# Kernel tuning notes

Measured on AMD Instinct MI355X. Metric: run time of the kernel, lower is better.

Reference implementation:

```python
import jax, jax.numpy as jnp
import numpy as np
from jax import lax

H = 64  # LSTM units (hard-coded in the module)


def _lstm(x, W, U, b, return_sequences):
    """Keras-style LSTM (inference; recurrent_dropout inactive).
    x: [B, T, F]; W: [F, 4H]; U: [H, 4H]; b: [4H].
    Gate order (Keras): i, f, g(cell), o.
    """
    B = x.shape[0]
    # Precompute input contribution for all timesteps: [T, B, 4H]
    xz = jnp.einsum('btf,fg->tbg', x, W) + b

    def step(carry, z_t):
        h, c = carry
        z = z_t + h @ U  # [B, 4H]
        i = jax.nn.sigmoid(z[:, :H])
        f = jax.nn.sigmoid(z[:, H:2 * H])
        g = jnp.tanh(z[:, 2 * H:3 * H])
        o = jax.nn.sigmoid(z[:, 3 * H:])
        c = f * c + i * g
        h = o * jnp.tanh(c)
        return (h, c), h

    init = (jnp.zeros((B, H), x.dtype), jnp.zeros((B, H), x.dtype))
    (h_last, _), hs = lax.scan(step, init, xz)
    if return_sequences:
        return jnp.transpose(hs, (1, 0, 2))  # [B, T, H]
    return h_last  # [B, H]


def setup_inputs() -> dict:
    key = jax.random.key(0)
    ks = jax.random.split(key, 8)
    B, T, F = 4096, 256, 32
    s_in = 1.0 / np.sqrt(F)
    s_h = 1.0 / np.sqrt(H)
    return {
        'x': jax.random.normal(ks[0], (B, T, F), jnp.float32),
        'W1': jax.random.normal(ks[1], (F, 4 * H), jnp.float32) * s_in,
        'U1': jax.random.normal(ks[2], (H, 4 * H), jnp.float32) * s_h,
        'b1': jnp.zeros((4 * H,), jnp.float32),
        'W2': jax.random.normal(ks[3], (H, 4 * H), jnp.float32) * s_h,
        'U2': jax.random.normal(ks[4], (H, 4 * H), jnp.float32) * s_h,
        'b2': jnp.zeros((4 * H,), jnp.float32),
        'Wd': jax.random.normal(ks[5], (H, H), jnp.float32) * s_h,
        'bd': jnp.zeros((H,), jnp.float32),
        'Wo': jax.random.normal(ks[6], (H, 1), jnp.float32) * s_h,
        'bo': jnp.zeros((1,), jnp.float32),
    }


def reference(x, W1, U1, b1, W2, U2, b2, Wd, bd, Wo, bo):
    h_seq = _lstm(x, W1, U1, b1, return_sequences=True)   # hidden_lstm
    h_last = _lstm(h_seq, W2, U2, b2, return_sequences=False)  # lstm_layer
    d = jax.nn.sigmoid(h_last @ Wd + bd)  # Dense(64, sigmoid)
    return jax.nn.sigmoid(d @ Wo + bo)    # Dense(1, sigmoid) -> [B, 1]
```

## Files before the change

kernel.cpp:

```cpp
#include <hip/hip_runtime.h>


typedef __attribute__((ext_vector_type(8))) short short8;
typedef __attribute__((ext_vector_type(4))) float floatx4;
typedef __attribute__((ext_vector_type(2))) float floatx2;

__device__ __forceinline__ float ex2(float x){ return __builtin_amdgcn_exp2f(x); }
__device__ __forceinline__ float rcp_(float x){ return __builtin_amdgcn_rcpf(x); }
__device__ __forceinline__ float sigm(float x){ return rcp_(1.0f + ex2(-1.44269504f*x)); }
__device__ __forceinline__ unsigned bfbits(float f){
    unsigned u = __builtin_bit_cast(unsigned, f);
    u += 0x7FFFu + ((u >> 16) & 1u);
    return u >> 16;
}
__device__ __forceinline__ short f2bf(float f){ return (short)bfbits(f); }
__device__ __forceinline__ unsigned pack_bf2(float a, float b){
    return bfbits(a) | (bfbits(b) << 16);
}

#define MFMA_BF16 __builtin_amdgcn_mfma_f32_16x16x32_bf16

__global__ __launch_bounds__(512, 1)
void lstm2_pipe(const float* __restrict__ x,
                const float* __restrict__ W1, const float* __restrict__ U1, const float* __restrict__ b1,
                const float* __restrict__ W2, const float* __restrict__ U2, const float* __restrict__ b2,
                const float* __restrict__ Wd, const float* __restrict__ bd,
                const float* __restrict__ Wo, const float* __restrict__ bo,
                float* __restrict__ out)
{
    __shared__ __align__(16) short h1b[2][16 * 72];
    __shared__ __align__(16) short h2b[2][16 * 72];
    __shared__ __align__(16) short xsb[2][16 * 40];
    __shared__ float psum[4][16];

    const int tid  = threadIdx.x;
    const int w    = tid >> 6;
    const bool isA = (w < 4);
    const int wv   = isA ? w : (w - 4);
    const int lane = tid & 63;
    const int m    = lane & 15;
    const int q    = lane >> 4;
    const int b0   = blockIdx.x * 16;
    const int col  = wv * 16 + m;

    const float LG  = 1.44269504f;

    short8 Wf[16];
    float  bg[4];
    if (isA) {
#pragma unroll
        for (int g = 0; g < 4; ++g) {
            const float s = (g == 2) ? (2.0f * LG) : (-LG);
            const int n = g * 64 + col;
            bg[g] = b1[n] * s;
#pragma unroll
            for (int j = 0; j < 8; ++j) {
                const int k = q * 8 + j;
                Wf[g * 3 + 0][j] = f2bf(W1[k * 256 + n] * s);
                Wf[g * 3 + 1][j] = f2bf(U1[k * 256 + n] * s);
                Wf[g * 3 + 2][j] = f2bf(U1[(32 + k) * 256 + n] * s);
            }
        }
    } else {
#pragma unroll
        for (int g = 0; g < 4; ++g) {
            const float s = (g == 2) ? (2.0f * LG) : (-LG);
            const int n = g * 64 + col;
            bg[g] = b2[n] * s;
#pragma unroll
            for (int j = 0; j < 8; ++j) {
                const int k = q * 8 + j;
                Wf[g * 4 + 0][j] = f2bf(W2[k * 256 + n] * s);
                Wf[g * 4 + 1][j] = f2bf(W2[(32 + k) * 256 + n] * s);
                Wf[g * 4 + 2][j] = f2bf(U2[k * 256 + n] * s);
                Wf[g * 4 + 3][j] = f2bf(U2[(32 + k) * 256 + n] * s);
            }
        }
    }

    {
        unsigned* p1 = (unsigned*)&h1b[0][0];
        unsigned* p2 = (unsigned*)&h2b[0][0];
        for (int i = tid; i < 1152; i += 512) { p1[i] = 0u; p2[i] = 0u; }
    }

    const int xr = tid >> 4;
    const int xc = (tid & 15) * 2;
    const float* xrow = x + (size_t)(b0 + xr) * 8192 + xc;
    floatx2 xv0;
    if (isA) {
        floatx2 v = *(const floatx2*)xrow;
        *(unsigned*)&xsb[0][xr * 40 + xc] = pack_bf2(v.x, v.y);
        xv0 = *(const floatx2*)(xrow + 32);
    }
    __syncthreads();

    float c[4] = {0, 0, 0, 0};

    for (int u = 0; u <= 256; ++u) {
        const int par = u & 1, pax = par ^ 1;
        if (isA) {
            if (u < 256) {
                short8 a0 = *(const short8*)&xsb[par][m * 40 + q * 8];
                short8 a1 = *(const short8*)&h1b[pax][m * 72 + q * 8];
                short8 a2 = *(const short8*)&h1b[pax][m * 72 + 32 + q * 8];
                floatx4 z[4];
#pragma unroll
                for (int g = 0; g < 4; ++g) {
                    floatx4 acc = { bg[g], bg[g], bg[g], bg[g] };
                    acc = MFMA_BF16(a0, Wf[g * 3 + 0], acc, 0, 0, 0);
                    acc = MFMA_BF16(a1, Wf[g * 3 + 1], acc, 0, 0, 0);
                    acc = MFMA_BF16(a2, Wf[g * 3 + 2], acc, 0, 0, 0);
                    z[g] = acc;
                }
                float hv[4];
#pragma unroll
                for (int r = 0; r < 4; ++r) {
                    float iv = rcp_(1.0f + ex2(z[0][r]));
                    float fv = rcp_(1.0f + ex2(z[1][r]));
                    float rg = rcp_(1.0f + ex2(z[2][r]));
                    float ov = rcp_(1.0f + ex2(z[3][r]));
                    float gp = fmaf(-5.77078016f, rg, 2.88539008f);
                    c[r] = fmaf(fv, c[r], iv * gp);
                    float th = fmaf(-2.0f, rcp_(1.0f + ex2(c[r])), 1.0f);
                    hv[r] = ov * th;
                }
                unsigned p01 = pack_bf2(hv[0], hv[1]);
                unsigned p23 = pack_bf2(hv[2], hv[3]);
                short* hw = &h1b[par][(q * 4) * 72 + col];
                hw[0]       = (short)(p01 & 0xFFFF);
                hw[72]      = (short)(p01 >> 16);
                hw[144]     = (short)(p23 & 0xFFFF);
                hw[216]     = (short)(p23 >> 16);
                if (u < 255) {
                    *(unsigned*)&xsb[pax][xr * 40 + xc] = pack_bf2(xv0.x, xv0.y);
                    if (u < 254) xv0 = *(const floatx2*)(xrow + (size_t)(u + 2) * 32);
                }
            }
        } else {
            if (u >= 1) {
                short8 g0 = *(const short8*)&h1b[pax][m * 72 + q * 8];
                short8 g1 = *(const short8*)&h1b[pax][m * 72 + 32 + q * 8];
                short8 g2 = *(const short8*)&h2b[par][m * 72 + q * 8];
                short8 g3 = *(const short8*)&h2b[par][m * 72 + 32 + q * 8];
                floatx4 z[4];
#pragma unroll
                for (int g = 0; g < 4; ++g) {
                    floatx4 acc = { bg[g], bg[g], bg[g], bg[g] };
                    acc = MFMA_BF16(g0, Wf[g * 4 + 0], acc, 0, 0, 0);
                    acc = MFMA_BF16(g1, Wf[g * 4 + 1], acc, 0, 0, 0);
                    acc = MFMA_BF16(g2, Wf[g * 4 + 2], acc, 0, 0, 0);
                    acc = MFMA_BF16(g3, Wf[g * 4 + 3], acc, 0, 0, 0);
                    z[g] = acc;
                }
                float hv[4];
#pragma unroll
                for (int r = 0; r < 4; ++r) {
                    float iv = rcp_(1.0f + ex2(z[0][r]));
                    float fv = rcp_(1.0f + ex2(z[1][r]));
                    float rg = rcp_(1.0f + ex2(z[2][r]));
                    float ov = rcp_(1.0f + ex2(z[3][r]));
                    float gp = fmaf(-5.77078016f, rg, 2.88539008f);
                    c[r] = fmaf(fv, c[r], iv * gp);
                    float th = fmaf(-2.0f, rcp_(1.0f + ex2(c[r])), 1.0f);
                    hv[r] = ov * th;
                }
                unsigned p01 = pack_bf2(hv[0], hv[1]);
                unsigned p23 = pack_bf2(hv[2], hv[3]);
                short* hw = &h2b[pax][(q * 4) * 72 + col];
                hw[0]       = (short)(p01 & 0xFFFF);
                hw[72]      = (short)(p01 >> 16);
                hw[144]     = (short)(p23 & 0xFFFF);
                hw[216]     = (short)(p23 >> 16);
            }
        }
        __syncthreads();
    }

    if (!isA) {
        short8 wd0, wd1;
#pragma unroll
        for (int j = 0; j < 8; ++j) {
            wd0[j] = f2bf(Wd[(q * 8 + j) * 64 + col] * (-LG));
            wd1[j] = f2bf(Wd[(32 + q * 8 + j) * 64 + col] * (-LG));
        }
        short8 hA0 = *(const short8*)&h2b[1][m * 72 + q * 8];
        short8 hA1 = *(const short8*)&h2b[1][m * 72 + 32 + q * 8];
        const float bdv = bd[col] * (-LG);
        floatx4 dacc = { bdv, bdv, bdv, bdv };
        dacc = MFMA_BF16(hA0, wd0, dacc, 0, 0, 0);
        dacc = MFMA_BF16(hA1, wd1, dacc, 0, 0, 0);
        const float wo = Wo[col];
#pragma unroll
        for (int r = 0; r < 4; ++r) {
            float p = rcp_(1.0f + ex2(dacc[r])) * wo;
            p += __shfl_xor(p, 1, 64);
            p += __shfl_xor(p, 2, 64);
            p += __shfl_xor(p, 4, 64);
            p += __shfl_xor(p, 8, 64);
            if (m == 0) psum[wv][q * 4 + r] = p;
        }
    }
    __syncthreads();
    if (tid >= 256 && tid < 272) {
        const int i = tid - 256;
        float s = psum[0][i] + psum[1][i] + psum[2][i] + psum[3][i] + bo[0];
        out[b0 + i] = sigm(s);
    }
}

extern "C" void kernel_launch(void* const* d_in, const int* in_sizes, int n_in,
                              void* d_out, int out_size, void* d_ws, size_t ws_size,
                              hipStream_t stream) {
    (void)in_sizes; (void)n_in; (void)d_ws; (void)ws_size; (void)out_size;
    const float* x  = (const float*)d_in[0];
    const float* W1 = (const float*)d_in[1];
    const float* U1 = (const float*)d_in[2];
    const float* b1 = (const float*)d_in[3];
    const float* W2 = (const float*)d_in[4];
    const float* U2 = (const float*)d_in[5];
    const float* b2 = (const float*)d_in[6];
    const float* Wd = (const float*)d_in[7];
    const float* bd = (const float*)d_in[8];
    const float* Wo = (const float*)d_in[9];
    const float* bo = (const float*)d_in[10];
    lstm2_pipe<<<dim3(256), dim3(512), 0, stream>>>(
        x, W1, U1, b1, W2, U2, b2, Wd, bd, Wo, bo, (float*)d_out);
}
```

Measured before the change: 356.0 us.

## Transpose gate MFMA layout and double waves per layer to 16 per block

Swaps the MFMA operand roles so the weights become the A operand and hidden states the B operand. Gate columns are interleaved so each lane's four accumulator rows hold the i, f, g and o gates of one unit, which removes the cross-row gate gathering. The block grows from 512 to 1024 threads, with 8 waves per LSTM layer each handling two 16-column tiles, halving the serial MFMA chain and per-thread activation work per step. The cost is more waves contending at the per-step barrier and scalar 2-byte LDS stores for h.

```diff
diff --git a/kernel.cpp b/kernel.cpp
--- a/kernel.cpp
+++ b/kernel.cpp
@@ -20,13 +20,13 @@
 
 #define MFMA_BF16 __builtin_amdgcn_mfma_f32_16x16x32_bf16
 
-__global__ __launch_bounds__(512, 1)
-void lstm2_pipe(const float* __restrict__ x,
-                const float* __restrict__ W1, const float* __restrict__ U1, const float* __restrict__ b1,
-                const float* __restrict__ W2, const float* __restrict__ U2, const float* __restrict__ b2,
-                const float* __restrict__ Wd, const float* __restrict__ bd,
-                const float* __restrict__ Wo, const float* __restrict__ bo,
-                float* __restrict__ out)
+__global__ __launch_bounds__(1024, 1)
+void lstm2_tz(const float* __restrict__ x,
+              const float* __restrict__ W1, const float* __restrict__ U1, const float* __restrict__ b1,
+              const float* __restrict__ W2, const float* __restrict__ U2, const float* __restrict__ b2,
+              const float* __restrict__ Wd, const float* __restrict__ bd,
+              const float* __restrict__ Wo, const float* __restrict__ bo,
+              float* __restrict__ out)
 {
     __shared__ __align__(16) short h1b[2][16 * 72];
     __shared__ __align__(16) short h2b[2][16 * 72];
@@ -35,162 +35,144 @@
 
     const int tid  = threadIdx.x;
     const int w    = tid >> 6;
-    const bool isA = (w < 4);
-    const int wv   = isA ? w : (w - 4);
+    const bool isL1 = (w < 8);
+    const int wv   = isL1 ? w : (w - 8);
     const int lane = tid & 63;
-    const int m    = lane & 15;
+    const int n    = lane & 15;
     const int q    = lane >> 4;
     const int b0   = blockIdx.x * 16;
-    const int col  = wv * 16 + m;
-
-    const float LG  = 1.44269504f;
-
-    short8 Wf[16];
-    float  bg[4];
-    if (isA) {
-#pragma unroll
-        for (int g = 0; g < 4; ++g) {
-            const float s = (g == 2) ? (2.0f * LG) : (-LG);
-            const int n = g * 64 + col;
-            bg[g] = b1[n] * s;
+
+    const float LG = 1.44269504f;
+
+    const int ugl = n >> 2;
+    const int gA  = n & 3;
+    const float sA = (gA == 2) ? (2.0f * LG) : (-LG);
+
+    short8  Wa[8];
+    floatx4 bC[2];
+    if (isL1) {
+#pragma unroll
+        for (int tt = 0; tt < 2; ++tt) {
+            const int t = wv * 2 + tt;
+            const int ncol = gA * 64 + t * 4 + ugl;
 #pragma unroll
             for (int j = 0; j < 8; ++j) {
                 const int k = q * 8 + j;
-                Wf[g * 3 + 0][j] = f2bf(W1[k * 256 + n] * s);
-                Wf[g * 3 + 1][j] = f2bf(U1[k * 256 + n] * s);
-                Wf[g * 3 + 2][j] = f2bf(U1[(32 + k) * 256 + n] * s);
-            }
+                Wa[tt * 3 + 0][j] = f2bf(W1[k * 256 + ncol] * sA);
+                Wa[tt * 3 + 1][j] = f2bf(U1[k * 256 + ncol] * sA);
+                Wa[tt * 3 + 2][j] = f2bf(U1[(32 + k) * 256 + ncol] * sA);
+            }
+#pragma unroll
+            for (int r = 0; r < 4; ++r)
+                bC[tt][r] = b1[r * 64 + t * 4 + q] * ((r == 2) ? (2.0f * LG) : (-LG));
         }
     } else {
 #pragma unroll
-        for (int g = 0; g < 4; ++g) {
-            const float s = (g == 2) ? (2.0f * LG) : (-LG);
-            const int n = g * 64 + col;
-            bg[g] = b2[n] * s;
+        for (int tt = 0; tt < 2; ++tt) {
+            const int t = wv * 2 + tt;
+            const int ncol = gA * 64 + t * 4 + ugl;
 #pragma unroll
             for (int j = 0; j < 8; ++j) {
                 const int k = q * 8 + j;
-                Wf[g * 4 + 0][j] = f2bf(W2[k * 256 + n] * s);
-                Wf[g * 4 + 1][j] = f2bf(W2[(32 + k) * 256 + n] * s);
-                Wf[g * 4 + 2][j] = f2bf(U2[k * 256 + n] * s);
-                Wf[g * 4 + 3][j] = f2bf(U2[(32 + k) * 256 + n] * s);
-            }
+                Wa[tt * 4 + 0][j] = f2bf(W2[k * 256 + ncol] * sA);
+                Wa[tt * 4 + 1][j] = f2bf(W2[(32 + k) * 256 + ncol] * sA);
+                Wa[tt * 4 + 2][j] = f2bf(U2[k * 256 + ncol] * sA);
+                Wa[tt * 4 + 3][j] = f2bf(U2[(32 + k) * 256 + ncol] * sA);
+            }
+#pragma unroll
+            for (int r = 0; r < 4; ++r)
+                bC[tt][r] = b2[r * 64 + t * 4 + q] * ((r == 2) ? (2.0f * LG) : (-LG));
         }
     }
 
     {
         unsigned* p1 = (unsigned*)&h1b[0][0];
         unsigned* p2 = (unsigned*)&h2b[0][0];
-        for (int i = tid; i < 1152; i += 512) { p1[i] = 0u; p2[i] = 0u; }
+        for (int i = tid; i < 1152; i += 1024) { p1[i] = 0u; p2[i] = 0u; }
     }
 
     const int xr = tid >> 4;
     const int xc = (tid & 15) * 2;
     const float* xrow = x + (size_t)(b0 + xr) * 8192 + xc;
     floatx2 xv0;
-    if (isA) {
+    if (tid < 256) {
         floatx2 v = *(const floatx2*)xrow;
         *(unsigned*)&xsb[0][xr * 40 + xc] = pack_bf2(v.x, v.y);
         xv0 = *(const floatx2*)(xrow + 32);
     }
     __syncthreads();
 
-    float c[4] = {0, 0, 0, 0};
+    float c[2] = {0, 0};
 
     for (int u = 0; u <= 256; ++u) {
         const int par = u & 1, pax = par ^ 1;
-        if (isA) {
+        if (isL1) {
             if (u < 256) {
-                short8 a0 = *(const short8*)&xsb[par][m * 40 + q * 8];
-                short8 a1 = *(const short8*)&h1b[pax][m * 72 + q * 8];
-                short8 a2 = *(const short8*)&h1b[pax][m * 72 + 32 + q * 8];
-                floatx4 z[4];
-#pragma unroll
-                for (int g = 0; g < 4; ++g) {
-                    floatx4 acc = { bg[g], bg[g], bg[g], bg[g] };
-                    acc = MFMA_BF16(a0, Wf[g * 3 + 0], acc, 0, 0, 0);
-                    acc = MFMA_BF16(a1, Wf[g * 3 + 1], acc, 0, 0, 0);
-                    acc = MFMA_BF16(a2, Wf[g * 3 + 2], acc, 0, 0, 0);
-                    z[g] = acc;
+                short8 bx  = *(const short8*)&xsb[par][n * 40 + q * 8];
+                short8 bh0 = *(const short8*)&h1b[pax][n * 72 + q * 8];
+                short8 bh1 = *(const short8*)&h1b[pax][n * 72 + 32 + q * 8];
+#pragma unroll
+                for (int tt = 0; tt < 2; ++tt) {
+                    floatx4 z = bC[tt];
+                    z = MFMA_BF16(Wa[tt * 3 + 0], bx,  z, 0, 0, 0);
+                    z = MFMA_BF16(Wa[tt * 3 + 1], bh0, z, 0, 0, 0);
+                    z = MFMA_BF16(Wa[tt * 3 + 2], bh1, z, 0, 0, 0);
+                    float iv = rcp_(1.0f + ex2(z[0]));
+                    float fv = rcp_(1.0f + ex2(z[1]));
+                    float rg = rcp_(1.0f + ex2(z[2]));
+                    float ov = rcp_(1.0f + ex2(z[3]));
+                    float gp = fmaf(-5.77078016f, rg, 2.88539008f);
+                    c[tt] = fmaf(fv, c[tt], iv * gp);
+                    float th = fmaf(-2.0f, rcp_(1.0f + ex2(c[tt])), 1.0f);
+                    h1b[par][n * 72 + (wv * 2 + tt) * 4 + q] = f2bf(ov * th);
                 }
-                float hv[4];
-#pragma unroll
-                for (int r = 0; r < 4; ++r) {
-                    float iv = rcp_(1.0f + ex2(z[0][r]));
-                    float fv = rcp_(1.0f + ex2(z[1][r]));
-                    float rg = rcp_(1.0f + ex2(z[2][r]));
-                    float ov = rcp_(1.0f + ex2(z[3][r]));
-                    float gp = fmaf(-5.77078016f, rg, 2.88539008f);
-                    c[r] = fmaf(fv, c[r], iv * gp);
-                    float th = fmaf(-2.0f, rcp_(1.0f + ex2(c[r])), 1.0f);
-                    hv[r] = ov * th;
-                }
-                unsigned p01 = pack_bf2(hv[0], hv[1]);
-                unsigned p23 = pack_bf2(hv[2], hv[3]);
-                short* hw = &h1b[par][(q * 4) * 72 + col];
-                hw[0]       = (short)(p01 & 0xFFFF);
-                hw[72]      = (short)(p01 >> 16);
-                hw[144]     = (short)(p23 & 0xFFFF);
-                hw[216]     = (short)(p23 >> 16);
-                if (u < 255) {
+                if (tid < 256 && u < 255) {
                     *(unsigned*)&xsb[pax][xr * 40 + xc] = pack_bf2(xv0.x, xv0.y);
                     if (u < 254) xv0 = *(const floatx2*)(xrow + (size_t)(u + 2) * 32);
                 }
             }
         } else {
             if (u >= 1) {
-                short8 g0 = *(const short8*)&h1b[pax][m * 72 + q * 8];
-                short8 g1 = *(const short8*)&h1b[pax][m * 72 + 32 + q * 8];
-                short8 g2 = *(const short8*)&h2b[par][m * 72 + q * 8];
-                short8 g3 = *(const short8*)&h2b[par][m * 72 + 32 + q * 8];
-                floatx4 z[4];
-#pragma unroll
-                for (int g = 0; g < 4; ++g) {
-                    floatx4 acc = { bg[g], bg[g], bg[g], bg[g] };
-                    acc = MFMA_BF16(g0, Wf[g * 4 + 0], acc, 0, 0, 0);
-                    acc = MFMA_BF16(g1, Wf[g * 4 + 1], acc, 0, 0, 0);
-                    acc = MFMA_BF16(g2, Wf[g * 4 + 2], acc, 0, 0, 0);
-                    acc = MFMA_BF16(g3, Wf[g * 4 + 3], acc, 0, 0, 0);
-                    z[g] = acc;
+                short8 bh0 = *(const short8*)&h1b[pax][n * 72 + q * 8];
+                short8 bh1 = *(const short8*)&h1b[pax][n * 72 + 32 + q * 8];
+                short8 bg0 = *(const short8*)&h2b[par][n * 72 + q * 8];
+                short8 bg1 = *(const short8*)&h2b[par][n * 72 + 32 + q * 8];
+#pragma unroll
+                for (int tt = 0; tt < 2; ++tt) {
+                    floatx4 z = bC[tt];
+                    z = MFMA_BF16(Wa[tt * 4 + 0], bh0, z, 0, 0, 0);
+                    z = MFMA_BF16(Wa[tt * 4 + 1], bh1, z, 0, 0, 0);
+                    z = MFMA_BF16(Wa[tt * 4 + 2], bg0, z, 0, 0, 0);
+                    z = MFMA_BF16(Wa[tt * 4 + 3], bg1, z, 0, 0, 0);
+                    float iv = rcp_(1.0f + ex2(z[0]));
+                    float fv = rcp_(1.0f + ex2(z[1]));
+                    float rg = rcp_(1.0f + ex2(z[2]));
+                    float ov = rcp_(1.0f + ex2(z[3]));
+                    float gp = fmaf(-5.77078016f, rg, 2.88539008f);
+                    c[tt] = fmaf(fv, c[tt], iv * gp);
+                    float th = fmaf(-2.0f, rcp_(1.0f + ex2(c[tt])), 1.0f);
+                    h2b[pax][n * 72 + (wv * 2 + tt) * 4 + q] = f2bf(ov * th);
                 }
-                float hv[4];
-#pragma unroll
-                for (int r = 0; r < 4; ++r) {
-                    float iv = rcp_(1.0f + ex2(z[0][r]));
-                    float fv = rcp_(1.0f + ex2(z[1][r]));
-                    float rg = rcp_(1.0f + ex2(z[2][r]));
-                    float ov = rcp_(1.0f + ex2(z[3][r]));
-                    float gp = fmaf(-5.77078016f, rg, 2.88539008f);
-                    c[r] = fmaf(fv, c[r], iv * gp);
-                    float th = fmaf(-2.0f, rcp_(1.0f + ex2(c[r])), 1.0f);
-                    hv[r] = ov * th;
-                }
-                unsigned p01 = pack_bf2(hv[0], hv[1]);
-                unsigned p23 = pack_bf2(hv[2], hv[3]);
-                short* hw = &h2b[pax][(q * 4) * 72 + col];
-                hw[0]       = (short)(p01 & 0xFFFF);
-                hw[72]      = (short)(p01 >> 16);
-                hw[144]     = (short)(p23 & 0xFFFF);
-                hw[216]     = (short)(p23 >> 16);
             }
         }
         __syncthreads();
     }
 
-    if (!isA) {
+    if (!isL1 && wv < 4) {
+        const int colD = wv * 16 + n;
         short8 wd0, wd1;
 #pragma unroll
         for (int j = 0; j < 8; ++j) {
-            wd0[j] = f2bf(Wd[(q * 8 + j) * 64 + col] * (-LG));
-            wd1[j] = f2bf(Wd[(32 + q * 8 + j) * 64 + col] * (-LG));
-        }
-        short8 hA0 = *(const short8*)&h2b[1][m * 72 + q * 8];
-        short8 hA1 = *(const short8*)&h2b[1][m * 72 + 32 + q * 8];
-        const float bdv = bd[col] * (-LG);
+            wd0[j] = f2bf(Wd[(q * 8 + j) * 64 + colD] * (-LG));
+            wd1[j] = f2bf(Wd[(32 + q * 8 + j) * 64 + colD] * (-LG));
+        }
+        short8 hA0 = *(const short8*)&h2b[1][n * 72 + q * 8];
+        short8 hA1 = *(const short8*)&h2b[1][n * 72 + 32 + q * 8];
+        const float bdv = bd[colD] * (-LG);
         floatx4 dacc = { bdv, bdv, bdv, bdv };
         dacc = MFMA_BF16(hA0, wd0, dacc, 0, 0, 0);
         dacc = MFMA_BF16(hA1, wd1, dacc, 0, 0, 0);
-        const float wo = Wo[col];
+        const float wo = Wo[colD];
 #pragma unroll
         for (int r = 0; r < 4; ++r) {
             float p = rcp_(1.0f + ex2(dacc[r])) * wo;
@@ -198,14 +180,13 @@
             p += __shfl_xor(p, 2, 64);
             p += __shfl_xor(p, 4, 64);
             p += __shfl_xor(p, 8, 64);
-            if (m == 0) psum[wv][q * 4 + r] = p;
+            if (n == 0) psum[wv][q * 4 + r] = p;
         }
     }
     __syncthreads();
-    if (tid >= 256 && tid < 272) {
-        const int i = tid - 256;
-        float s = psum[0][i] + psum[1][i] + psum[2][i] + psum[3][i] + bo[0];
-        out[b0 + i] = sigm(s);
+    if (tid < 16) {
+        float s = psum[0][tid] + psum[1][tid] + psum[2][tid] + psum[3][tid] + bo[0];
+        out[b0 + tid] = sigm(s);
     }
 }
 
@@ -224,6 +205,6 @@
     const float* bd = (const float*)d_in[8];
     const float* Wo = (const float*)d_in[9];
     const float* bo = (const float*)d_in[10];
-    lstm2_pipe<<<dim3(256), dim3(512), 0, stream>>>(
+    lstm2_tz<<<dim3(256), dim3(1024), 0, stream>>>(
         x, W1, U1, b1, W2, U2, b2, Wd, bd, Wo, bo, (float*)d_out);
 }
```

Result: faster. 343.7 us (-3.5%).
